# Optimization experiments

Measured on AMD Instinct MI355X. Metric: run time of the kernel, lower is better.

The kernel has to match this reference:

```python
import jax, jax.numpy as jnp
import numpy as np

C, H, W = 8, 2048, 2048
NUM_SEG = 64      # labels 0..63; label 0 = background (ndimage.label convention)
SIGMA_AGG = 0.5


def setup_inputs() -> dict:
    key = jax.random.key(0)
    k1, k2, k3 = jax.random.split(key, 3)
    pred_similarities = jax.random.normal(k1, (C, H, W), dtype=jnp.float32)
    kernel_labels = jax.random.randint(k2, (H, W), 0, NUM_SEG).astype(jnp.int32)
    region_labels = jax.random.randint(k3, (H, W), 0, NUM_SEG).astype(jnp.int32)
    # masks are 1 exactly where a connected component exists (labels > 0),
    # matching what ndimage.label would produce from these masks
    kernels_mask = (kernel_labels > 0).astype(jnp.float32)
    regions_mask = (region_labels > 0).astype(jnp.float32)
    return {
        "pred_similarities": pred_similarities,
        "regions_mask": regions_mask,
        "kernels_mask": kernels_mask,
        "kernel_labels": kernel_labels,
        "region_labels": region_labels,
    }


def reference(pred_similarities, regions_mask, kernels_mask, kernel_labels, region_labels):
    h, w = kernel_labels.shape
    kl = kernel_labels.reshape(-1)  # [N]
    rl = region_labels.reshape(-1)  # [N]

    # per-label cardinality, broadcast back to pixels (label 0 contributes 0
    # because the mask is 0 there, matching the original's untouched zeros)
    kcard = jax.ops.segment_sum(kernels_mask.reshape(-1), kl, num_segments=NUM_SEG)[kl].reshape(h, w)
    rcard = jax.ops.segment_sum(regions_mask.reshape(-1), rl, num_segments=NUM_SEG)[rl].reshape(h, w)

    # per-channel, per-kernel-component sum of pred, broadcast back per pixel
    c = pred_similarities.shape[0]
    pred_flat = pred_similarities.reshape(c, -1)  # [C, N]
    seg = jax.vmap(lambda p: jax.ops.segment_sum(p, kl, num_segments=NUM_SEG))(pred_flat)  # [C, NUM_SEG]
    Gk = jnp.where(kl[None, :] > 0, seg[:, kl], 0.0).reshape(c, h, w)
    Gk = Gk / (kcard + 1.0)[None]

    Fp = pred_similarities * regions_mask[None]
    diff = Fp - Gk
    # torch.linalg.norm over the whole tensor -> scalar Frobenius norm
    D = jnp.maximum(jnp.sqrt(jnp.sum(diff * diff)) - SIGMA_AGG, 0.0)
    per_pixel = jnp.log(D * D + 1.0) / (rcard + 1.0)  # [H, W]

    num_region = jnp.maximum(jnp.max(region_labels), 1).astype(per_pixel.dtype)
    return jnp.sum(per_pixel) / num_region
```

## Files before the change

### kernel.cpp

```cpp
#include <hip/hip_runtime.h>
#include <math.h>

#define NPIX (2048*2048)
#define NBLOCKS 1024
#define CHUNK (NPIX/NBLOCKS)
#define SPX 256
#define NSTEP (CHUNK/SPX)
#define PSTR 260
#define KOFF (8*PSTR)
#define ROFF (KOFF+SPX)
#define SBUF (ROFF+SPX)

#define WS_T1 1024
#define WS_T2 2048
#define WS_F2 2304
#define WS_FLOATS 2305
#define L_T1 1088
#define L_T2 2176
#define LDS_RED (2176 + 16*17)

typedef __attribute__((ext_vector_type(8))) short short8;
typedef __attribute__((ext_vector_type(4))) float f32x4;
typedef __attribute__((ext_vector_type(4))) unsigned int u32x4;

typedef __attribute__((address_space(3))) unsigned int lds_uint;
typedef __attribute__((address_space(1))) unsigned int glb_uint;

#define WAITVM(n) __builtin_amdgcn_s_waitcnt(0x0F70 | (n))

__device__ __forceinline__ unsigned int pk_trunc_bf16(float lo, float hi) {
    return __builtin_amdgcn_perm(__float_as_uint(hi), __float_as_uint(lo), 0x07060302u);
}
__device__ __forceinline__ unsigned int pk_lab(int lo, int hi) {
    return __builtin_amdgcn_perm((unsigned)hi, (unsigned)lo, 0x05040100u);
}
__device__ __forceinline__ unsigned int onehot2(unsigned int x, unsigned int tp) {
    const unsigned int a = x ^ tp;
    const unsigned int t = 0x40004000u - a;
    return t & 0x40004000u;
}

__device__ __forceinline__ void dma1k(const void* g, void* l, int lane) {
    __builtin_amdgcn_global_load_lds(
        (const glb_uint*)((const char*)g + lane * 16),
        (lds_uint*)l, 16, 0, 0);
}

__device__ __forceinline__ void issue_dma(int wv, int lane, float* base, int P,
                                          const float* pred, const int* kl,
                                          const int* rl) {
    dma1k(pred + (size_t)wv * NPIX + P,      base + wv * PSTR,      lane);
    dma1k(pred + (size_t)(wv + 4) * NPIX + P, base + (wv + 4) * PSTR, lane);
    if (wv == 0) dma1k(kl + P, base + KOFF, lane);
    if (wv == 1) dma1k(rl + P, base + ROFF, lane);
}

__global__ __launch_bounds__(256, 4) void agg_mfma(
    const float* __restrict__ pred,
    const int*   __restrict__ kl,
    const int*   __restrict__ rl,
    float* __restrict__ ws)
{
    __shared__ union {
        float stage[2][SBUF];
        float red[LDS_RED];
    } sh;
    __shared__ float s_f2w[4];

    const int tid  = threadIdx.x;
    const int wv   = tid >> 6;
    const int lane = tid & 63;
    const int quad = lane >> 4;
    const int col  = lane & 15;
    const int c8   = col & 7;
    const bool lowcol = (col < 8);
    const unsigned int cpack = (unsigned)col * 0x00010001u;
    const unsigned int tps[4] = {cpack, cpack + 0x00100010u,
                                 cpack + 0x00200020u, cpack + 0x00300030u};
    const unsigned int hc = (col == 8) ? 0x3F803F80u : 0u;
    const short8 b2c = __builtin_bit_cast(short8, (u32x4){hc, hc, hc, hc});

    f32x4 acc0[4], acc1[4], acc2;
    #pragma unroll
    for (int s = 0; s < 4; ++s) {
        acc0[s] = (f32x4){0.f, 0.f, 0.f, 0.f};
        acc1[s] = (f32x4){0.f, 0.f, 0.f, 0.f};
    }
    acc2 = (f32x4){0.f, 0.f, 0.f, 0.f};
    float f2 = 0.f;

    const int P0 = blockIdx.x * CHUNK;
    issue_dma(wv, lane, sh.stage[0], P0, pred, kl, rl);

    for (int s = 0; s < NSTEP; ++s) {
        const int par = s & 1;
        if (s + 1 < NSTEP)
            issue_dma(wv, lane, sh.stage[par ^ 1], P0 + (s + 1) * SPX, pred, kl, rl);
        if (s + 1 < NSTEP) { if (wv < 2) WAITVM(3); else WAITVM(2); }
        else WAITVM(0);
        __builtin_amdgcn_s_barrier();

        const float* base = sh.stage[par];
        #pragma unroll
        for (int i = 0; i < 2; ++i) {
            const int pb = (2 * wv + i) * 32 + quad * 8;
            const int* kptr = (const int*)(base + KOFF) + pb;
            const int* rptr = (const int*)(base + ROFF) + pb;
            const float* pptr = base + c8 * PSTR + pb;
            const int4 ka = *(const int4*)kptr;
            const int4 kb = *(const int4*)(kptr + 4);
            const int4 ra = *(const int4*)rptr;
            const int4 rb = *(const int4*)(rptr + 4);
            const float4 pa = *(const float4*)pptr;
            const float4 pb4 = *(const float4*)(pptr + 4);

            const int   klv[8] = {ka.x, ka.y, ka.z, ka.w, kb.x, kb.y, kb.z, kb.w};
            const int   rlv[8] = {ra.x, ra.y, ra.z, ra.w, rb.x, rb.y, rb.z, rb.w};
            const float pv[8]  = {pa.x, pa.y, pa.z, pa.w, pb4.x, pb4.y, pb4.z, pb4.w};

            float pr[8];
            #pragma unroll
            for (int j = 0; j < 8; ++j) {
                pr[j] = (rlv[j] > 0) ? pv[j] : 0.f;
                f2 = fmaf(pr[j], pr[j], f2);
            }
            unsigned int b1p[4], kp[4], rp[4];
            #pragma unroll
            for (int q = 0; q < 4; ++q) {
                const int j0 = 2 * q, j1 = 2 * q + 1;
                const unsigned int plo = pk_trunc_bf16(pv[j0], pv[j1]);
                const unsigned int phi = pk_trunc_bf16(pr[j0], pr[j1]);
                b1p[q] = lowcol ? plo : phi;
                kp[q]  = pk_lab(klv[j0], klv[j1]);
                rp[q]  = pk_lab(rlv[j0], rlv[j1]);
            }
            const short8 b1 = __builtin_bit_cast(short8,
                (u32x4){b1p[0], b1p[1], b1p[2], b1p[3]});

            #pragma unroll
            for (int t = 0; t < 4; ++t) {
                u32x4 oh;
                #pragma unroll
                for (int q = 0; q < 4; ++q) oh[q] = onehot2(kp[q], tps[t]);
                const short8 ak = __builtin_bit_cast(short8, oh);
                acc0[t] = __builtin_amdgcn_mfma_f32_16x16x32_bf16(ak, b1,  acc0[t], 0, 0, 0);
                acc1[t] = __builtin_amdgcn_mfma_f32_16x16x32_bf16(ak, b2c, acc1[t], 0, 0, 0);
            }
            u32x4 alo, bhi;
            #pragma unroll
            for (int q = 0; q < 4; ++q) {
                alo[q] = onehot2(rp[q] & 0x000F000Fu, cpack);
                bhi[q] = onehot2((rp[q] >> 4) & 0x00030003u, cpack);
            }
            acc2 = __builtin_amdgcn_mfma_f32_16x16x32_bf16(
                __builtin_bit_cast(short8, alo), __builtin_bit_cast(short8, bhi),
                acc2, 0, 0, 0);
        }
        __builtin_amdgcn_s_barrier();
    }

    #pragma unroll
    for (int off = 32; off > 0; off >>= 1) f2 += __shfl_down(f2, off, 64);
    if (lane == 0) s_f2w[wv] = f2;

    __syncthreads();
    for (int w = 0; w < 4; ++w) {
        if (wv == w) {
            #pragma unroll
            for (int t = 0; t < 4; ++t)
                #pragma unroll
                for (int i = 0; i < 4; ++i) {
                    const int l = t * 16 + quad * 4 + i;
                    const int a0 = l * 17 + col;
                    const int a1 = L_T1 + l * 17 + col;
                    if (w == 0) { sh.red[a0] = acc0[t][i]; sh.red[a1] = acc1[t][i]; }
                    else        { sh.red[a0] += acc0[t][i]; sh.red[a1] += acc1[t][i]; }
                }
            #pragma unroll
            for (int i = 0; i < 4; ++i) {
                const int a2 = L_T2 + (quad * 4 + i) * 17 + col;
                if (w == 0) sh.red[a2] = acc2[i]; else sh.red[a2] += acc2[i];
            }
        }
        __syncthreads();
    }
    if (tid == 0)
        atomicAdd(&ws[WS_F2], s_f2w[0] + s_f2w[1] + s_f2w[2] + s_f2w[3]);
    for (int idx = tid; idx < 2304; idx += 256) {
        int a;
        if (idx < 1024)      a = (idx >> 4) * 17 + (idx & 15);
        else if (idx < 2048) a = L_T1 + ((idx - 1024) >> 4) * 17 + (idx & 15);
        else                 a = L_T2 + ((idx - 2048) >> 4) * 17 + (idx & 15);
        atomicAdd(&ws[idx], sh.red[a]);
    }
}

__global__ __launch_bounds__(64) void agg_final(const float* __restrict__ ws,
                                                float* __restrict__ out)
{
    const int l = threadIdx.x;
    const float* t0 = ws + l * 16;
    const float pck = 0.5f  * ws[WS_T1 + l * 16 + 8];
    const float pcr = 0.25f * ws[WS_T2 + (l & 15) * 16 + (l >> 4)];

    float corr = 0.f;
    if (l > 0) {
        #pragma unroll
        for (int c = 0; c < 8; ++c) {
            const float seg = 0.5f * t0[c];
            const float T   = 0.5f * t0[8 + c];
            const float gk  = seg / (pck + 1.f);
            corr += gk * (gk * pck - 2.f * T);
        }
    }
    const float rcard = (l > 0) ? pcr : 0.f;
    float S = pcr / (rcard + 1.f);
    int mx = (pcr > 0.5f) ? l : 0;
    float f2 = (l == 0) ? 0.5f * ws[WS_F2] : 0.f;

    #pragma unroll
    for (int off = 32; off > 0; off >>= 1) {
        f2   += __shfl_down(f2, off, 64);
        corr += __shfl_down(corr, off, 64);
        S    += __shfl_down(S, off, 64);
        mx    = max(mx, __shfl_down(mx, off, 64));
    }
    if (l == 0) {
        const float SS = f2 + corr;
        float D = sqrtf(fmaxf(SS, 0.f)) - 0.5f;
        D = fmaxf(D, 0.f);
        out[0] = logf(D * D + 1.f) * S / (float)max(mx, 1);
    }
}

extern "C" void kernel_launch(void* const* d_in, const int* in_sizes, int n_in,
                              void* d_out, int out_size, void* d_ws, size_t ws_size,
                              hipStream_t stream) {
    const float* pred = (const float*)d_in[0];
    const int* kl = (const int*)d_in[3];
    const int* rl = (const int*)d_in[4];
    float* ws = (float*)d_ws;

    hipMemsetAsync(d_ws, 0, WS_FLOATS * sizeof(float), stream);
    agg_mfma<<<NBLOCKS, 256, 0, stream>>>(pred, kl, rl, ws);
    agg_final<<<1, 64, 0, stream>>>(ws, (float*)d_out);
}
```

Before: 262.6 us.

## Compute kernel-label counts via outer-product MFMA and grid-stride over more blocks

Kernel-label cardinality is now computed with a single 16x4 one-hot outer-product MFMA, the same trick already used for region counts, instead of four MFMAs against a constant column. That removes four accumulators and three MFMAs per sub-step and shrinks the reduction workspace and shared-memory footprint. The grid also switches from fixed contiguous chunks to a grid-stride loop over 1536 blocks, with launch bounds raised to 6 blocks per SM for more occupancy. The final kernel's read of the kernel count changes to match the new layout, and there is a register-pressure risk from the higher occupancy target.

```diff
diff --git a/kernel.cpp b/kernel.cpp
--- a/kernel.cpp
+++ b/kernel.cpp
@@ -2,22 +2,21 @@
 #include <math.h>
 
 #define NPIX (2048*2048)
-#define NBLOCKS 1024
-#define CHUNK (NPIX/NBLOCKS)
 #define SPX 256
-#define NSTEP (CHUNK/SPX)
+#define TSTEPS (NPIX/SPX)
+#define NBLOCKS 1536
 #define PSTR 260
 #define KOFF (8*PSTR)
 #define ROFF (KOFF+SPX)
 #define SBUF (ROFF+SPX)
 
 #define WS_T1 1024
-#define WS_T2 2048
-#define WS_F2 2304
-#define WS_FLOATS 2305
+#define WS_T2 1280
+#define WS_F2 1536
+#define WS_FLOATS 1537
 #define L_T1 1088
-#define L_T2 2176
-#define LDS_RED (2176 + 16*17)
+#define L_T2 1360
+#define LDS_RED 1632
 
 typedef __attribute__((ext_vector_type(8))) short short8;
 typedef __attribute__((ext_vector_type(4))) float f32x4;
@@ -49,13 +48,13 @@
 __device__ __forceinline__ void issue_dma(int wv, int lane, float* base, int P,
                                           const float* pred, const int* kl,
                                           const int* rl) {
-    dma1k(pred + (size_t)wv * NPIX + P,      base + wv * PSTR,      lane);
+    dma1k(pred + (size_t)wv * NPIX + P,       base + wv * PSTR,       lane);
     dma1k(pred + (size_t)(wv + 4) * NPIX + P, base + (wv + 4) * PSTR, lane);
     if (wv == 0) dma1k(kl + P, base + KOFF, lane);
     if (wv == 1) dma1k(rl + P, base + ROFF, lane);
 }
 
-__global__ __launch_bounds__(256, 4) void agg_mfma(
+__global__ __launch_bounds__(256, 6) void agg_mfma(
     const float* __restrict__ pred,
     const int*   __restrict__ kl,
     const int*   __restrict__ rl,
@@ -77,26 +76,23 @@
     const unsigned int cpack = (unsigned)col * 0x00010001u;
     const unsigned int tps[4] = {cpack, cpack + 0x00100010u,
                                  cpack + 0x00200020u, cpack + 0x00300030u};
-    const unsigned int hc = (col == 8) ? 0x3F803F80u : 0u;
-    const short8 b2c = __builtin_bit_cast(short8, (u32x4){hc, hc, hc, hc});
-
-    f32x4 acc0[4], acc1[4], acc2;
+
+    f32x4 acc0[4], acc1, acc2;
     #pragma unroll
-    for (int s = 0; s < 4; ++s) {
-        acc0[s] = (f32x4){0.f, 0.f, 0.f, 0.f};
-        acc1[s] = (f32x4){0.f, 0.f, 0.f, 0.f};
-    }
+    for (int s = 0; s < 4; ++s) acc0[s] = (f32x4){0.f, 0.f, 0.f, 0.f};
+    acc1 = (f32x4){0.f, 0.f, 0.f, 0.f};
     acc2 = (f32x4){0.f, 0.f, 0.f, 0.f};
     float f2 = 0.f;
 
-    const int P0 = blockIdx.x * CHUNK;
-    issue_dma(wv, lane, sh.stage[0], P0, pred, kl, rl);
-
-    for (int s = 0; s < NSTEP; ++s) {
-        const int par = s & 1;
-        if (s + 1 < NSTEP)
-            issue_dma(wv, lane, sh.stage[par ^ 1], P0 + (s + 1) * SPX, pred, kl, rl);
-        if (s + 1 < NSTEP) { if (wv < 2) WAITVM(3); else WAITVM(2); }
+    int s = blockIdx.x;
+    int par = 0;
+    issue_dma(wv, lane, sh.stage[0], s * SPX, pred, kl, rl);
+
+    while (true) {
+        const int sn = s + NBLOCKS;
+        const bool more = (sn < TSTEPS);
+        if (more) issue_dma(wv, lane, sh.stage[par ^ 1], sn * SPX, pred, kl, rl);
+        if (more) { if (wv < 2) WAITVM(3); else WAITVM(2); }
         else WAITVM(0);
         __builtin_amdgcn_s_barrier();
 
@@ -142,11 +138,18 @@
                 u32x4 oh;
                 #pragma unroll
                 for (int q = 0; q < 4; ++q) oh[q] = onehot2(kp[q], tps[t]);
-                const short8 ak = __builtin_bit_cast(short8, oh);
-                acc0[t] = __builtin_amdgcn_mfma_f32_16x16x32_bf16(ak, b1,  acc0[t], 0, 0, 0);
-                acc1[t] = __builtin_amdgcn_mfma_f32_16x16x32_bf16(ak, b2c, acc1[t], 0, 0, 0);
+                acc0[t] = __builtin_amdgcn_mfma_f32_16x16x32_bf16(
+                    __builtin_bit_cast(short8, oh), b1, acc0[t], 0, 0, 0);
             }
             u32x4 alo, bhi;
+            #pragma unroll
+            for (int q = 0; q < 4; ++q) {
+                alo[q] = onehot2(kp[q] & 0x000F000Fu, cpack);
+                bhi[q] = onehot2((kp[q] >> 4) & 0x00030003u, cpack);
+            }
+            acc1 = __builtin_amdgcn_mfma_f32_16x16x32_bf16(
+                __builtin_bit_cast(short8, alo), __builtin_bit_cast(short8, bhi),
+                acc1, 0, 0, 0);
             #pragma unroll
             for (int q = 0; q < 4; ++q) {
                 alo[q] = onehot2(rp[q] & 0x000F000Fu, cpack);
@@ -157,6 +160,8 @@
                 acc2, 0, 0, 0);
         }
         __builtin_amdgcn_s_barrier();
+        if (!more) break;
+        s = sn; par ^= 1;
     }
 
     #pragma unroll
@@ -172,25 +177,25 @@
                 for (int i = 0; i < 4; ++i) {
                     const int l = t * 16 + quad * 4 + i;
                     const int a0 = l * 17 + col;
-                    const int a1 = L_T1 + l * 17 + col;
-                    if (w == 0) { sh.red[a0] = acc0[t][i]; sh.red[a1] = acc1[t][i]; }
-                    else        { sh.red[a0] += acc0[t][i]; sh.red[a1] += acc1[t][i]; }
+                    if (w == 0) sh.red[a0] = acc0[t][i]; else sh.red[a0] += acc0[t][i];
                 }
             #pragma unroll
             for (int i = 0; i < 4; ++i) {
+                const int a1 = L_T1 + (quad * 4 + i) * 17 + col;
                 const int a2 = L_T2 + (quad * 4 + i) * 17 + col;
-                if (w == 0) sh.red[a2] = acc2[i]; else sh.red[a2] += acc2[i];
+                if (w == 0) { sh.red[a1] = acc1[i]; sh.red[a2] = acc2[i]; }
+                else        { sh.red[a1] += acc1[i]; sh.red[a2] += acc2[i]; }
             }
         }
         __syncthreads();
     }
     if (tid == 0)
         atomicAdd(&ws[WS_F2], s_f2w[0] + s_f2w[1] + s_f2w[2] + s_f2w[3]);
-    for (int idx = tid; idx < 2304; idx += 256) {
+    for (int idx = tid; idx < 1536; idx += 256) {
         int a;
         if (idx < 1024)      a = (idx >> 4) * 17 + (idx & 15);
-        else if (idx < 2048) a = L_T1 + ((idx - 1024) >> 4) * 17 + (idx & 15);
-        else                 a = L_T2 + ((idx - 2048) >> 4) * 17 + (idx & 15);
+        else if (idx < 1280) a = L_T1 + ((idx - 1024) >> 4) * 17 + (idx & 15);
+        else                 a = L_T2 + ((idx - 1280) >> 4) * 17 + (idx & 15);
         atomicAdd(&ws[idx], sh.red[a]);
     }
 }
@@ -200,7 +205,7 @@
 {
     const int l = threadIdx.x;
     const float* t0 = ws + l * 16;
-    const float pck = 0.5f  * ws[WS_T1 + l * 16 + 8];
+    const float pck = 0.25f * ws[WS_T1 + (l & 15) * 16 + (l >> 4)];
     const float pcr = 0.25f * ws[WS_T2 + (l & 15) * 16 + (l >> 4)];
 
     float corr = 0.f;
```

Measured after the change: 264.1 us. No clear change (+0.6%).
